# Kernel tuning notes

Hardware: AMD Instinct MI355X
Metric: run time of the kernel (lower is better)

The kernel has to match this reference:

```python
import jax, jax.numpy as jnp
import numpy as np

IT = 3  # BP iterations
ROWS, N = 144, 576  # H dims: wman_N0576_R34 -> 144 checks, 576 vars
ROW_DEG = 6  # check-node degree


def _make_H():
    rng = np.random.default_rng(0)
    H = np.zeros((ROWS, N), np.float32)
    for i in range(ROWS):
        cols = rng.choice(N, size=ROW_DEG, replace=False)
        H[i, cols] = 1.0
    return jnp.asarray(H)


def _quantize(x, eta, qk):
    # 4-level soft quantization: softmax over -(x-qk)^2/(2 eta^2)
    logits = -(x[..., None] - qk) ** 2 / (2.0 * eta ** 2 + 1e-12)
    w = jax.nn.softmax(logits, axis=-1)
    return jnp.sum(w * qk, axis=-1)


def setup_inputs() -> dict:
    key = jax.random.key(0)
    k1, = jax.random.split(key, 1)
    batch = 512
    r = jax.random.normal(k1, (batch, N), dtype=jnp.float32)
    H = _make_H()
    alpha = jnp.ones((IT,), jnp.float32) * 0.7
    beta = jnp.ones((IT,), jnp.float32) * 0.05
    eta = jnp.ones((IT,), jnp.float32) * 0.7
    qk = jnp.linspace(-4.0, 4.0, 4).astype(jnp.float32)
    return {"r": r, "H": H, "alpha": alpha, "beta": beta, "eta": eta, "qk": qk}


def reference(r, H, alpha, beta, eta, qk):
    B, n = r.shape
    Hmask = H == 1
    node_idx = jnp.arange(n)[None, None, :]
    M = H[None] * r[:, None, :]          # (B, ROWS, N)
    E = jnp.zeros_like(M)
    for t in range(IT):
        # --- check-to-variable (min-sum with masked top-2) ---
        masked_abs = jnp.where(Hmask, jnp.abs(M), jnp.inf)
        neg_top, idx = jax.lax.top_k(-masked_abs, 2)  # two smallest
        min1 = -neg_top[..., 0:1]
        min2 = -neg_top[..., 1:2]
        idx1 = idx[..., 0:1]
        E_abs = jnp.where(node_idx == idx1, min2, min1)
        signs = jnp.sign(M)
        valid_signs = jnp.where(Hmask, signs, 1.0)
        row_sign_prod = jnp.prod(valid_signs, axis=2, keepdims=True)
        E_sign = row_sign_prod * valid_signs
        E = alpha[t] * E_sign * jnp.maximum(0.0, E_abs - beta[t])
        E = E * H
        E = _quantize(E, eta[t], qk)
        # --- variable-to-check update ---
        sum_E = jnp.sum(E, axis=1, keepdims=True)
        M = (r[:, None, :] + sum_E - E) * H[None]
        M = _quantize(M, eta[t], qk)
    return r + jnp.sum(E, axis=1)
```

## Files before the change

### kernel.cpp

```cpp
#include <hip/hip_runtime.h>
#include <math.h>

#define IT 3
#define ROWS 144
#define NCOLS 576
#define ROW_DEG 6
#define FLAG_OFF (ROWS * ROW_DEG)
#define MAGIC 0x3C96A51B

__device__ __forceinline__ float quantize1(float x, float S,
                                           float K0, float K1,
                                           float KQ0, float KQ1) {
    float s = fminf(fmaxf(x * S, -30.0f), 30.0f);
    float B = __expf(s);
    float den = ((K0 * B + K1) * B + K1) * B + K0;
    float num = (((-KQ0) * B + (-KQ1)) * B + KQ1) * B + KQ0;
    return num * __builtin_amdgcn_rcpf(den);
}

__device__ __forceinline__ float signf(float x) {
    return (x > 0.0f) ? 1.0f : ((x < 0.0f) ? -1.0f : 0.0f);
}

__global__ __launch_bounds__(64) void fused_kernel(
    const float* __restrict__ r, const float* __restrict__ H,
    const float* __restrict__ alpha, const float* __restrict__ beta,
    const float* __restrict__ eta, const float* __restrict__ qk,
    int* __restrict__ ws, float* __restrict__ out)
{
    int* cols  = ws;
    int* flags = ws + FLAG_OFF;
    const int lane = threadIdx.x;

    if (blockIdx.x < ROWS) {
        const int row = blockIdx.x;
        float hv[9];
        #pragma unroll
        for (int i = 0; i < 9; ++i) hv[i] = H[row * NCOLS + i * 64 + lane];

        int base = 0;
        #pragma unroll
        for (int i = 0; i < 9; ++i) {
            bool nz = hv[i] != 0.0f;
            unsigned long long mask = __ballot(nz);
            if (nz) {
                int rank = base + __popcll(mask & ((1ull << lane) - 1ull));
                if (rank < ROW_DEG) cols[row * ROW_DEG + rank] = i * 64 + lane;
            }
            base += __popcll(mask);
        }

        __threadfence();
        if (lane == 0) atomicExch(&flags[row], MAGIC);
        return;
    }

    __shared__ __align__(16) float s_r[NCOLS];
    __shared__ __align__(16) float s_sum[2][NCOLS];

    const int b = blockIdx.x - ROWS;

    const float4* rb4 = reinterpret_cast<const float4*>(r + (size_t)b * NCOLS);
    float4* s_r4 = reinterpret_cast<float4*>(s_r);
    #pragma unroll
    for (int p = 0; p < 3; ++p) {
        int j = lane + 64 * p;
        if (j < NCOLS / 4) s_r4[j] = rb4[j];
    }
    #pragma unroll
    for (int p = 0; p < 9; ++p) s_sum[0][lane + 64 * p] = 0.0f;

    const float q0 = qk[0], q1 = qk[1], q3 = qk[3];
    const float dq = (q3 - q0) * (1.0f / 3.0f);
    float S_[IT], A_[IT], Be_[IT], K0_[IT], K1_[IT], KQ0_[IT], KQ1_[IT];
    #pragma unroll
    for (int t = 0; t < IT; ++t) {
        float et = eta[t];
        float i2e = 1.0f / (2.0f * et * et + 1e-12f);
        S_[t]   = 2.0f * dq * i2e;
        A_[t]   = alpha[t];
        Be_[t]  = beta[t];
        K0_[t]  = __expf(-q0 * q0 * i2e);
        K1_[t]  = __expf(-q1 * q1 * i2e);
        KQ0_[t] = K0_[t] * q0;
        KQ1_[t] = K1_[t] * q1;
    }

    {
        const int f0 = lane, f1 = lane + 64;
        const int f2 = (lane + 128 < ROWS) ? (lane + 128) : 0;
        for (;;) {
            int a0 = __hip_atomic_load(&flags[f0], __ATOMIC_RELAXED,
                                       __HIP_MEMORY_SCOPE_AGENT);
            int a1 = __hip_atomic_load(&flags[f1], __ATOMIC_RELAXED,
                                       __HIP_MEMORY_SCOPE_AGENT);
            int a2 = __hip_atomic_load(&flags[f2], __ATOMIC_RELAXED,
                                       __HIP_MEMORY_SCOPE_AGENT);
            if (__all((a0 == MAGIC) & (a1 == MAGIC) & (a2 == MAGIC))) break;
            __builtin_amdgcn_s_sleep(8);
        }
        (void)__hip_atomic_load(&flags[0], __ATOMIC_ACQUIRE,
                                __HIP_MEMORY_SCOPE_AGENT);
    }

    const bool act2 = lane < (ROWS - 128);

    int c[3][ROW_DEG];
    #pragma unroll
    for (int p = 0; p < 3; ++p) {
        if (p == 2 && !act2) continue;
        const int row = lane + 64 * p;
        #pragma unroll
        for (int e = 0; e < ROW_DEG; ++e)
            c[p][e] = __hip_atomic_load(&cols[row * ROW_DEG + e],
                                        __ATOMIC_RELAXED,
                                        __HIP_MEMORY_SCOPE_AGENT);
    }

    __syncthreads();

    float rc[3][ROW_DEG], m[3][ROW_DEG], E[3][ROW_DEG];
    #pragma unroll
    for (int p = 0; p < 3; ++p) {
        if (p == 2 && !act2) continue;
        #pragma unroll
        for (int e = 0; e < ROW_DEG; ++e) {
            rc[p][e] = s_r[c[p][e]];
            m[p][e]  = rc[p][e];
        }
    }

    #pragma unroll
    for (int t = 0; t < IT; ++t) {
        const int cur = t & 1, nxt = cur ^ 1;
        const float S = S_[t], A = A_[t], Bt = Be_[t];
        const float K0 = K0_[t], K1 = K1_[t], KQ0 = KQ0_[t], KQ1 = KQ1_[t];

        #pragma unroll
        for (int p = 0; p < 3; ++p) {
            if (p == 2 && !act2) continue;
            float min1 = INFINITY, min2 = INFINITY;
            int idx = -1;
            float sp = 1.0f;
            #pragma unroll
            for (int e = 0; e < ROW_DEG; ++e) {
                float a = fabsf(m[p][e]);
                sp *= signf(m[p][e]);
                if (a < min1) { min2 = min1; min1 = a; idx = e; }
                else if (a < min2) { min2 = a; }
            }
            float qf1 = quantize1(A * sp * fmaxf(0.0f, min1 - Bt), S, K0, K1, KQ0, KQ1);
            float qf2 = quantize1(A * sp * fmaxf(0.0f, min2 - Bt), S, K0, K1, KQ0, KQ1);
            #pragma unroll
            for (int e = 0; e < ROW_DEG; ++e) {
                float v = signf(m[p][e]) * ((e == idx) ? qf2 : qf1);
                E[p][e] = v;
                atomicAdd(&s_sum[cur][c[p][e]], v);
            }
        }
        __syncthreads();

        if (t < IT - 1) {
            #pragma unroll
            for (int p = 0; p < 9; ++p) s_sum[nxt][lane + 64 * p] = 0.0f;
            #pragma unroll
            for (int p = 0; p < 3; ++p) {
                if (p == 2 && !act2) continue;
                #pragma unroll
                for (int e = 0; e < ROW_DEG; ++e) {
                    float v = rc[p][e] + s_sum[cur][c[p][e]] - E[p][e];
                    m[p][e] = quantize1(v, S, K0, K1, KQ0, KQ1);
                }
            }
            __syncthreads();
        }
    }

    float4* ob4 = reinterpret_cast<float4*>(out + (size_t)b * NCOLS);
    const float4* s_s4 = reinterpret_cast<const float4*>(s_sum[0]);
    #pragma unroll
    for (int p = 0; p < 3; ++p) {
        int j = lane + 64 * p;
        if (j < NCOLS / 4) {
            float4 rv = s_r4[j], sv = s_s4[j];
            float4 o;
            o.x = rv.x + sv.x; o.y = rv.y + sv.y;
            o.z = rv.z + sv.z; o.w = rv.w + sv.w;
            ob4[j] = o;
        }
    }
}

extern "C" void kernel_launch(void* const* d_in, const int* in_sizes, int n_in,
                              void* d_out, int out_size, void* d_ws, size_t ws_size,
                              hipStream_t stream) {
    const float* r     = (const float*)d_in[0];
    const float* H     = (const float*)d_in[1];
    const float* alpha = (const float*)d_in[2];
    const float* beta  = (const float*)d_in[3];
    const float* eta   = (const float*)d_in[4];
    const float* qk    = (const float*)d_in[5];
    float* out = (float*)d_out;

    const int batch = in_sizes[0] / NCOLS;

    hipLaunchKernelGGL(fused_kernel, dim3(ROWS + batch), dim3(64), 0, stream,
                       r, H, alpha, beta, eta, qk, (int*)d_ws, out);
}
```

Before: 87.88 us.

## Build H column table per block in LDS, drop cross-block flag spin-wait

Removes the separate producer blocks that extracted H's nonzero columns into global workspace, and the flag-polling spin-wait that consumer blocks used to wait for them. Each 512-thread block now handles 8 batch items, one per wave. The 8 waves together scan all 144 H rows into a shared column table before a single block barrier. Per-iteration __syncthreads become __threadfence_block since each wave owns its own LDS sum buffers. Every block now re-reads all of H (about 330KB), and larger LDS use per block may limit occupancy.

```diff
diff --git a/kernel.cpp b/kernel.cpp
--- a/kernel.cpp
+++ b/kernel.cpp
@@ -5,8 +5,9 @@
 #define ROWS 144
 #define NCOLS 576
 #define ROW_DEG 6
-#define FLAG_OFF (ROWS * ROW_DEG)
-#define MAGIC 0x3C96A51B
+#define NW 8
+#define NT (NW * 64)
+#define ROWS_PER_WAVE (ROWS / NW)
 
 __device__ __forceinline__ float quantize1(float x, float S,
                                            float K0, float K1,
@@ -22,22 +23,36 @@
     return (x > 0.0f) ? 1.0f : ((x < 0.0f) ? -1.0f : 0.0f);
 }
 
-__global__ __launch_bounds__(64) void fused_kernel(
+__global__ __launch_bounds__(NT) void fused_kernel(
     const float* __restrict__ r, const float* __restrict__ H,
     const float* __restrict__ alpha, const float* __restrict__ beta,
     const float* __restrict__ eta, const float* __restrict__ qk,
-    int* __restrict__ ws, float* __restrict__ out)
+    float* __restrict__ out, int batch)
 {
-    int* cols  = ws;
-    int* flags = ws + FLAG_OFF;
-    const int lane = threadIdx.x;
+    __shared__ __align__(16) float s_r[NW][NCOLS];
+    __shared__ __align__(16) float s_sum[NW][2][NCOLS];
+    __shared__ int s_cols[ROWS * ROW_DEG];
 
-    if (blockIdx.x < ROWS) {
-        const int row = blockIdx.x;
+    const int tid  = threadIdx.x;
+    const int w    = tid >> 6;
+    const int lane = tid & 63;
+    const int b    = blockIdx.x * NW + w;
+    const bool live = b < batch;
+    const int bsafe = live ? b : 0;
+
+    const float4* rb4 = reinterpret_cast<const float4*>(r + (size_t)bsafe * NCOLS);
+    float4 rv[3];
+    #pragma unroll
+    for (int p = 0; p < 3; ++p) {
+        int j = lane + 64 * p;
+        if (j < NCOLS / 4) rv[p] = rb4[j];
+    }
+
+    for (int k = 0; k < ROWS_PER_WAVE; ++k) {
+        const int row = w + NW * k;
         float hv[9];
         #pragma unroll
         for (int i = 0; i < 9; ++i) hv[i] = H[row * NCOLS + i * 64 + lane];
-
         int base = 0;
         #pragma unroll
         for (int i = 0; i < 9; ++i) {
@@ -45,30 +60,20 @@
             unsigned long long mask = __ballot(nz);
             if (nz) {
                 int rank = base + __popcll(mask & ((1ull << lane) - 1ull));
-                if (rank < ROW_DEG) cols[row * ROW_DEG + rank] = i * 64 + lane;
+                if (rank < ROW_DEG) s_cols[row * ROW_DEG + rank] = i * 64 + lane;
             }
             base += __popcll(mask);
         }
-
-        __threadfence();
-        if (lane == 0) atomicExch(&flags[row], MAGIC);
-        return;
     }
 
-    __shared__ __align__(16) float s_r[NCOLS];
-    __shared__ __align__(16) float s_sum[2][NCOLS];
-
-    const int b = blockIdx.x - ROWS;
-
-    const float4* rb4 = reinterpret_cast<const float4*>(r + (size_t)b * NCOLS);
-    float4* s_r4 = reinterpret_cast<float4*>(s_r);
+    float4* s_r4 = reinterpret_cast<float4*>(s_r[w]);
     #pragma unroll
     for (int p = 0; p < 3; ++p) {
         int j = lane + 64 * p;
-        if (j < NCOLS / 4) s_r4[j] = rb4[j];
+        if (j < NCOLS / 4) s_r4[j] = rv[p];
     }
     #pragma unroll
-    for (int p = 0; p < 9; ++p) s_sum[0][lane + 64 * p] = 0.0f;
+    for (int p = 0; p < 9; ++p) s_sum[w][0][lane + 64 * p] = 0.0f;
 
     const float q0 = qk[0], q1 = qk[1], q3 = qk[3];
     const float dq = (q3 - q0) * (1.0f / 3.0f);
@@ -86,22 +91,9 @@
         KQ1_[t] = K1_[t] * q1;
     }
 
-    {
-        const int f0 = lane, f1 = lane + 64;
-        const int f2 = (lane + 128 < ROWS) ? (lane + 128) : 0;
-        for (;;) {
-            int a0 = __hip_atomic_load(&flags[f0], __ATOMIC_RELAXED,
-                                       __HIP_MEMORY_SCOPE_AGENT);
-            int a1 = __hip_atomic_load(&flags[f1], __ATOMIC_RELAXED,
-                                       __HIP_MEMORY_SCOPE_AGENT);
-            int a2 = __hip_atomic_load(&flags[f2], __ATOMIC_RELAXED,
-                                       __HIP_MEMORY_SCOPE_AGENT);
-            if (__all((a0 == MAGIC) & (a1 == MAGIC) & (a2 == MAGIC))) break;
-            __builtin_amdgcn_s_sleep(8);
-        }
-        (void)__hip_atomic_load(&flags[0], __ATOMIC_ACQUIRE,
-                                __HIP_MEMORY_SCOPE_AGENT);
-    }
+    __syncthreads();
+
+    if (!live) return;
 
     const bool act2 = lane < (ROWS - 128);
 
@@ -111,13 +103,8 @@
         if (p == 2 && !act2) continue;
         const int row = lane + 64 * p;
         #pragma unroll
-        for (int e = 0; e < ROW_DEG; ++e)
-            c[p][e] = __hip_atomic_load(&cols[row * ROW_DEG + e],
-                                        __ATOMIC_RELAXED,
-                                        __HIP_MEMORY_SCOPE_AGENT);
+        for (int e = 0; e < ROW_DEG; ++e) c[p][e] = s_cols[row * ROW_DEG + e];
     }
-
-    __syncthreads();
 
     float rc[3][ROW_DEG], m[3][ROW_DEG], E[3][ROW_DEG];
     #pragma unroll
@@ -125,7 +112,7 @@
         if (p == 2 && !act2) continue;
         #pragma unroll
         for (int e = 0; e < ROW_DEG; ++e) {
-            rc[p][e] = s_r[c[p][e]];
+            rc[p][e] = s_r[w][c[p][e]];
             m[p][e]  = rc[p][e];
         }
     }
@@ -155,37 +142,37 @@
             for (int e = 0; e < ROW_DEG; ++e) {
                 float v = signf(m[p][e]) * ((e == idx) ? qf2 : qf1);
                 E[p][e] = v;
-                atomicAdd(&s_sum[cur][c[p][e]], v);
+                atomicAdd(&s_sum[w][cur][c[p][e]], v);
             }
         }
-        __syncthreads();
+        __threadfence_block();
 
         if (t < IT - 1) {
             #pragma unroll
-            for (int p = 0; p < 9; ++p) s_sum[nxt][lane + 64 * p] = 0.0f;
+            for (int p = 0; p < 9; ++p) s_sum[w][nxt][lane + 64 * p] = 0.0f;
             #pragma unroll
             for (int p = 0; p < 3; ++p) {
                 if (p == 2 && !act2) continue;
                 #pragma unroll
                 for (int e = 0; e < ROW_DEG; ++e) {
-                    float v = rc[p][e] + s_sum[cur][c[p][e]] - E[p][e];
+                    float v = rc[p][e] + s_sum[w][cur][c[p][e]] - E[p][e];
                     m[p][e] = quantize1(v, S, K0, K1, KQ0, KQ1);
                 }
             }
-            __syncthreads();
+            __threadfence_block();
         }
     }
 
     float4* ob4 = reinterpret_cast<float4*>(out + (size_t)b * NCOLS);
-    const float4* s_s4 = reinterpret_cast<const float4*>(s_sum[0]);
+    const float4* s_s4 = reinterpret_cast<const float4*>(s_sum[w][0]);
     #pragma unroll
     for (int p = 0; p < 3; ++p) {
         int j = lane + 64 * p;
         if (j < NCOLS / 4) {
-            float4 rv = s_r4[j], sv = s_s4[j];
+            float4 rvv = s_r4[j], sv = s_s4[j];
             float4 o;
-            o.x = rv.x + sv.x; o.y = rv.y + sv.y;
-            o.z = rv.z + sv.z; o.w = rv.w + sv.w;
+            o.x = rvv.x + sv.x; o.y = rvv.y + sv.y;
+            o.z = rvv.z + sv.z; o.w = rvv.w + sv.w;
             ob4[j] = o;
         }
     }
@@ -202,8 +189,11 @@
     const float* qk    = (const float*)d_in[5];
     float* out = (float*)d_out;
 
-    const int batch = in_sizes[0] / NCOLS;
+    const int batch  = in_sizes[0] / NCOLS;
+    const int blocks = (batch + NW - 1) / NW;
 
-    hipLaunchKernelGGL(fused_kernel, dim3(ROWS + batch), dim3(64), 0, stream,
-                       r, H, alpha, beta, eta, qk, (int*)d_ws, out);
+    (void)d_ws; (void)ws_size;
+
+    hipLaunchKernelGGL(fused_kernel, dim3(blocks), dim3(NT), 0, stream,
+                       r, H, alpha, beta, eta, qk, out, batch);
 }
```

Result: slower. 106.8 us (+21.5%).
